# Kernel optimization log

Measured on AMD Instinct MI355X. Metric: run time of the kernel, lower is better.

## Reference

```python
import jax, jax.numpy as jnp
import numpy as np

SEQ_LEN = 2048
EMBED = 1024
HIDDEN = 64
BATCH = 8


def setup_inputs() -> dict:
    key = jax.random.key(0)
    ks = jax.random.split(key, 7)
    s = 1.0 / np.sqrt(EMBED)
    return {
        "inputs": jax.random.normal(ks[0], (BATCH, SEQ_LEN, EMBED), dtype=jnp.float32),
        "Wq": jax.random.uniform(ks[1], (EMBED, HIDDEN), jnp.float32, -s, s),
        "bq": jax.random.uniform(ks[2], (HIDDEN,), jnp.float32, -s, s),
        "Wk": jax.random.uniform(ks[3], (EMBED, HIDDEN), jnp.float32, -s, s),
        "bk": jax.random.uniform(ks[4], (HIDDEN,), jnp.float32, -s, s),
        "Wv": jax.random.uniform(ks[5], (EMBED, HIDDEN), jnp.float32, -s, s),
        "bv": jax.random.uniform(ks[6], (HIDDEN,), jnp.float32, -s, s),
    }


def reference(inputs, Wq, bq, Wk, bk, Wv, bv):
    # inputs: [B, T, E]
    q = inputs @ Wq + bq  # [B, T, H]
    k = inputs @ Wk + bk
    v = inputs @ Wv + bv
    scale = 1.0 / jnp.sqrt(jnp.asarray(k.shape[-1], q.dtype))
    scores = jnp.einsum("bqh,bkh->bqk", q, k) * scale  # [B, T, T]
    T = scores.shape[1]
    tril = jnp.tril(jnp.ones((T, T), dtype=scores.dtype))
    # NOTE: multiplicative mask (zeros out future scores) exactly as in the torch module,
    # NOT an additive -inf mask.
    scores = scores * tril
    attn = jax.nn.softmax(scores, axis=-1)
    return jnp.einsum("bqk,bkh->bqh", attn, v)  # [B, T, H]
```

## Files before the change

kernel.cpp:

```cpp
#include <hip/hip_runtime.h>

#define NBATCH 8
#define TSEQ 2048
#define EDIM 1024
#define HDIM 64
#define NROW (NBATCH * TSEQ)

typedef unsigned short u16;
typedef __attribute__((ext_vector_type(8))) short bf16x8;
typedef __attribute__((ext_vector_type(8))) short short8;
typedef __attribute__((ext_vector_type(4))) float f32x4;

typedef unsigned int uint_as1 __attribute__((address_space(1)));
typedef unsigned int uint_as3 __attribute__((address_space(3)));

__device__ __forceinline__ u16 f2b(float x) {
  unsigned int u = __float_as_uint(x);
  unsigned int r = (u + 0x7fffu + ((u >> 16) & 1u)) >> 16;
  return (u16)r;
}
__device__ __forceinline__ float b2f(u16 h) {
  return __uint_as_float(((unsigned int)h) << 16);
}
__device__ __forceinline__ void gl16(const void* g, void* l) {
  __builtin_amdgcn_global_load_lds((const uint_as1*)g, (uint_as3*)l, 16, 0, 0);
}

__global__ __launch_bounds__(256) void wt_kernel(
    const float* __restrict__ Wq, const float* __restrict__ Wk,
    const float* __restrict__ Wv, u16* __restrict__ Wt) {
  __shared__ float s[64][65];
  const int o = blockIdx.x >> 4, et = blockIdx.x & 15;
  const float* W = (o == 0) ? Wq : (o == 1) ? Wk : Wv;
  const int t = threadIdx.x;
  const int e0 = et * 64;
#pragma unroll
  for (int i = 0; i < 16; i++) {
    int e = i * 4 + (t >> 6), h = t & 63;
    s[e][h] = W[(size_t)(e0 + e) * HDIM + h];
  }
  __syncthreads();
#pragma unroll
  for (int j = 0; j < 16; j++) {
    int h = j * 4 + (t >> 6), e = t & 63;
    Wt[(size_t)(o * 64 + h) * EDIM + e0 + e] = f2b(s[e][h]);
  }
}

#define XBUF (32 * 256)
#define WBUF (192 * 128)

__global__ __launch_bounds__(256, 2) void proj_mfma(
    const float* __restrict__ X, const u16* __restrict__ Wt,
    const float* __restrict__ bq, const float* __restrict__ bk,
    const float* __restrict__ bv,
    u16* __restrict__ Qb, u16* __restrict__ Kb, u16* __restrict__ Vt) {
  __shared__ __align__(16) char sx[2 * XBUF];
  __shared__ __align__(16) char sw[2 * WBUF];

  const int tid = threadIdx.x;
  const int w = tid >> 6, l = tid & 63;
  const int g = l >> 4, li = l & 15;
  const long bt0 = (long)blockIdx.x * 32;

  const int xr = tid >> 4, xc = tid & 15;
  const float* xsrc0 = X + (bt0 + xr) * EDIM + ((xc ^ (xr & 7)) * 4);
  const float* xsrc1 = X + (bt0 + 16 + xr) * EDIM + ((xc ^ (xr & 7)) * 4);

  f32x4 acc[6];
#pragma unroll
  for (int i = 0; i < 6; i++) acc[i] = (f32x4)0.f;

#define STAGE(BUF, E0)                                                       \
  do {                                                                       \
    gl16(xsrc0 + (E0), sx + (BUF)*XBUF + tid * 16);                          \
    gl16(xsrc1 + (E0), sx + (BUF)*XBUF + (tid + 256) * 16);                  \
    _Pragma("unroll") for (int j = 0; j < 6; j++) {                          \
      const int L = j * 256 + tid;                                           \
      const int r = L >> 3, c = L & 7;                                       \
      gl16(Wt + (size_t)r * EDIM + (E0) + ((c ^ (r & 7)) * 8),               \
           sw + (BUF)*WBUF + L * 16);                                        \
    }                                                                        \
  } while (0)

  STAGE(0, 0);
  asm volatile("s_waitcnt vmcnt(0)" ::: "memory");
  __builtin_amdgcn_sched_barrier(0);
  __builtin_amdgcn_s_barrier();
  __builtin_amdgcn_sched_barrier(0);

  for (int ks = 0; ks < 16; ks++) {
    const int buf = ks & 1;
    if (ks < 15) STAGE(buf ^ 1, (ks + 1) * 64);
    __builtin_amdgcn_sched_barrier(0);
    if (ks < 15) {
      asm volatile("s_waitcnt vmcnt(8)" ::: "memory");
    } else {
      asm volatile("s_waitcnt vmcnt(0)" ::: "memory");
    }
    __builtin_amdgcn_sched_barrier(0);
    __builtin_amdgcn_s_barrier();
    __builtin_amdgcn_sched_barrier(0);

    const char* xb = sx + buf * XBUF;
    const char* wb = sw + buf * WBUF;
    bf16x8 bfr[2][2];
#pragma unroll
    for (int cs = 0; cs < 2; cs++) {
      const int row = cs * 16 + li;
#pragma unroll
      for (int kc = 0; kc < 2; kc++) {
        const int G0 = kc * 8 + g * 2;
        const float4 f0 = *(const float4*)(xb + row * 256 + ((G0 ^ (row & 7)) * 16));
        const float4 f1 = *(const float4*)(xb + row * 256 + (((G0 + 1) ^ (row & 7)) * 16));
        bfr[cs][kc] = (bf16x8){(short)f2b(f0.x), (short)f2b(f0.y),
                               (short)f2b(f0.z), (short)f2b(f0.w),
                               (short)f2b(f1.x), (short)f2b(f1.y),
                               (short)f2b(f1.z), (short)f2b(f1.w)};
      }
    }
#pragma unroll
    for (int mt = 0; mt < 3; mt++) {
      const int row = w * 48 + mt * 16 + li;
#pragma unroll
      for (int kc = 0; kc < 2; kc++) {
        const int G = kc * 4 + g;
        const bf16x8 af = *(const bf16x8*)(wb + row * 128 + ((G ^ (row & 7)) * 16));
        acc[mt * 2 + 0] = __builtin_amdgcn_mfma_f32_16x16x32_bf16(
            af, bfr[0][kc], acc[mt * 2 + 0], 0, 0, 0);
        acc[mt * 2 + 1] = __builtin_amdgcn_mfma_f32_16x16x32_bf16(
            af, bfr[1][kc], acc[mt * 2 + 1], 0, 0, 0);
      }
    }
    __builtin_amdgcn_sched_barrier(0);
    __builtin_amdgcn_s_barrier();
    __builtin_amdgcn_sched_barrier(0);
  }
#undef STAGE

  const float qscale = 0.18033688011112042f;
#pragma unroll
  for (int cs = 0; cs < 2; cs++) {
    const long tg = bt0 + cs * 16 + li;
    const int b = (int)(tg >> 11), tl = (int)(tg & 2047);
#pragma unroll
    for (int mt = 0; mt < 3; mt++) {
      const int n0 = w * 48 + mt * 16 + g * 4;
      const int o = n0 >> 6;
      const int h0 = n0 & 63;
      const float* bias = (o == 0) ? bq : (o == 1) ? bk : bv;
      const float4 bb = *(const float4*)&bias[h0];
      const f32x4 a = acc[mt * 2 + cs];
      float v0 = a.x + bb.x, v1 = a.y + bb.y;
      float v2 = a.z + bb.z, v3 = a.w + bb.w;
      if (o == 0) {
        v0 *= qscale; v1 *= qscale; v2 *= qscale; v3 *= qscale;
        uint2 pk = make_uint2((unsigned)f2b(v0) | ((unsigned)f2b(v1) << 16),
                              (unsigned)f2b(v2) | ((unsigned)f2b(v3) << 16));
        *(uint2*)&Qb[tg * HDIM + h0] = pk;
      } else if (o == 1) {
        uint2 pk = make_uint2((unsigned)f2b(v0) | ((unsigned)f2b(v1) << 16),
                              (unsigned)f2b(v2) | ((unsigned)f2b(v3) << 16));
        *(uint2*)&Kb[tg * HDIM + h0] = pk;
      } else {
        Vt[(size_t)(b * 64 + h0 + 0) * TSEQ + tl] = f2b(v0);
        Vt[(size_t)(b * 64 + h0 + 1) * TSEQ + tl] = f2b(v1);
        Vt[(size_t)(b * 64 + h0 + 2) * TSEQ + tl] = f2b(v2);
        Vt[(size_t)(b * 64 + h0 + 3) * TSEQ + tl] = f2b(v3);
      }
    }
  }
}

__global__ __launch_bounds__(1024) void css_kernel(const u16* __restrict__ Vt,
                                                   float* __restrict__ CSS) {
  __shared__ float cs[32][64];
  const int b = blockIdx.x;
  const int t = threadIdx.x;
  const int h = t & 63, cg = t >> 6;
  const u16* vp = Vt + ((size_t)b * 64 + h) * TSEQ + cg * 128;
  float s0 = 0.f, s1 = 0.f;
#pragma unroll
  for (int i = 0; i < 8; i++) {
    const short8 a = *(const short8*)(vp + i * 8);
    s0 += b2f((u16)a[0]) + b2f((u16)a[1]) + b2f((u16)a[2]) + b2f((u16)a[3]) +
          b2f((u16)a[4]) + b2f((u16)a[5]) + b2f((u16)a[6]) + b2f((u16)a[7]);
  }
#pragma unroll
  for (int i = 8; i < 16; i++) {
    const short8 a = *(const short8*)(vp + i * 8);
    s1 += b2f((u16)a[0]) + b2f((u16)a[1]) + b2f((u16)a[2]) + b2f((u16)a[3]) +
          b2f((u16)a[4]) + b2f((u16)a[5]) + b2f((u16)a[6]) + b2f((u16)a[7]);
  }
  cs[cg * 2 + 0][h] = s0;
  cs[cg * 2 + 1][h] = s1;
  __syncthreads();
  if (t < 64) {
    float S = 0.f;
    CSS[((size_t)b * 33 + 32) * 64 + t] = 0.f;
    for (int c = 31; c >= 0; c--) {
      S += cs[c][t];
      CSS[((size_t)b * 33 + c) * 64 + t] = S;
    }
  }
}

#define ISSUE_K(K0A, K1A, KO)                                              \
  do {                                                                     \
    _Pragma("unroll") for (int n = 0; n < 4; n++) {                        \
      const u16* kp_ = Kbb + (size_t)((KO) + n * 16 + li) * HDIM + g * 8;  \
      K0A[n] = *(const bf16x8*)(kp_);                                      \
      K1A[n] = *(const bf16x8*)(kp_ + 32);                                 \
    }                                                                      \
  } while (0)

#define ISSUE_V(KO)                                                        \
  do {                                                                     \
    _Pragma("unroll") for (int n = 0; n < 4; n++) {                        \
      const u16* vp_ = Vtb + (size_t)(n * 16 + li) * TSEQ + (KO) + g * 8;  \
      vf0[n] = *(const bf16x8*)(vp_);                                      \
      vf1[n] = *(const bf16x8*)(vp_ + 32);                                 \
    }                                                                      \
  } while (0)

#define COMPUTE_TILE(K0A, K1A, KO)                                         \
  do {                                                                     \
    f32x4 sA_[4], sB_[4];                                                  \
    _Pragma("unroll") for (int n = 0; n < 4; n++) {                        \
      sA_[n] = (f32x4)0.f;                                                 \
      sA_[n] = __builtin_amdgcn_mfma_f32_16x16x32_bf16(K0A[n], qa0[0], sA_[n], 0, 0, 0); \
      sA_[n] = __builtin_amdgcn_mfma_f32_16x16x32_bf16(K1A[n], qa0[1], sA_[n], 0, 0, 0); \
      sB_[n] = (f32x4)0.f;                                                 \
      sB_[n] = __builtin_amdgcn_mfma_f32_16x16x32_bf16(K0A[n], qa1[0], sB_[n], 0, 0, 0); \
      sB_[n] = __builtin_amdgcn_mfma_f32_16x16x32_bf16(K1A[n], qa1[1], sB_[n], 0, 0, 0); \
    }                                                                      \
    _Pragma("unroll") for (int n = 0; n < 4; n++) {                        \
      const int kb_ = (KO) + n * 16 + g * 4;                               \
      float p0_ = (kb_ + 0 <= qiL0) ? exp2f(sA_[n][0]) : 1.0f;             \
      float p1_ = (kb_ + 1 <= qiL0) ? exp2f(sA_[n][1]) : 1.0f;             \
      float p2_ = (kb_ + 2 <= qiL0) ? exp2f(sA_[n][2]) : 1.0f;             \
      float p3_ = (kb_ + 3 <= qiL0) ? exp2f(sA_[n][3]) : 1.0f;             \
      zaccA += (p0_ + p1_) + (p2_ + p3_);                                  \
      uint2 pk_ = make_uint2((unsigned)f2b(p0_) | ((unsigned)f2b(p1_) << 16), \
                             (unsigned)f2b(p2_) | ((unsigned)f2b(p3_) << 16)); \
      *(uint2*)(sppw + li * 144 + n * 32 + g * 8) = pk_;                   \
      float q0_ = (kb_ + 0 <= qiL1) ? exp2f(sB_[n][0]) : 1.0f;             \
      float q1_ = (kb_ + 1 <= qiL1) ? exp2f(sB_[n][1]) : 1.0f;             \
      float q2_ = (kb_ + 2 <= qiL1) ? exp2f(sB_[n][2]) : 1.0f;             \
      float q3_ = (kb_ + 3 <= qiL1) ? exp2f(sB_[n][3]) : 1.0f;             \
      zaccB += (q0_ + q1_) + (q2_ + q3_);                                  \
      uint2 qk_ = make_uint2((unsigned)f2b(q0_) | ((unsigned)f2b(q1_) << 16), \
                             (unsigned)f2b(q2_) | ((unsigned)f2b(q3_) << 16)); \
      *(uint2*)(sppw + (li + 16) * 144 + n * 32 + g * 8) = qk_;            \
    }                                                                      \
    asm volatile("s_waitcnt lgkmcnt(0)" ::: "memory");                     \
    __builtin_amdgcn_sched_barrier(0);                                     \
    const bf16x8 paA0_ = *(const bf16x8*)(sppw + li * 144 + g * 16);       \
    const bf16x8 paA1_ = *(const bf16x8*)(sppw + li * 144 + 64 + g * 16);  \
    const bf16x8 paB0_ = *(const bf16x8*)(sppw + (li + 16) * 144 + g * 16);\
    const bf16x8 paB1_ = *(const bf16x8*)(sppw + (li + 16) * 144 + 64 + g * 16); \
    _Pragma("unroll") for (int nt = 0; nt < 4; nt++) {                     \
      oaccA[nt] = __builtin_amdgcn_mfma_f32_16x16x32_bf16(paA0_, vf0[nt], oaccA[nt], 0, 0, 0); \
      oaccA[nt] = __builtin_amdgcn_mfma_f32_16x16x32_bf16(paA1_, vf1[nt], oaccA[nt], 0, 0, 0); \
      oaccB[nt] = __builtin_amdgcn_mfma_f32_16x16x32_bf16(paB0_, vf0[nt], oaccB[nt], 0, 0, 0); \
      oaccB[nt] = __builtin_amdgcn_mfma_f32_16x16x32_bf16(paB1_, vf1[nt], oaccB[nt], 0, 0, 0); \
    }                                                                      \
  } while (0)

__global__ __launch_bounds__(256, 2) void attn_mfma(
    const u16* __restrict__ Qb, const u16* __restrict__ Kb,
    const u16* __restrict__ Vt, const float* __restrict__ CSS,
    float* __restrict__ Out) {
  __shared__ __align__(16) u16 spp[4][32][72];
  __shared__ float spm[4][32][68];

  const int tid = threadIdx.x;
  const int w = tid >> 6, l = tid & 63;
  const int g = l >> 4, li = l & 15;

  const int gb = blockIdx.x & 7;
  const int j = blockIdx.x >> 3;
  const int gr = 63 - j;
  const int q0 = gr * 32;
  const int qiL0 = q0 + li;
  const int qiL1 = q0 + 16 + li;

  char* sppw = (char*)&spp[w][0][0];

  const size_t qbase0 = ((size_t)gb * TSEQ + q0 + li) * HDIM;
  bf16x8 qa0[2], qa1[2];
  qa0[0] = *(const bf16x8*)(Qb + qbase0 + g * 8);
  qa0[1] = *(const bf16x8*)(Qb + qbase0 + g * 8 + 32);
  qa1[0] = *(const bf16x8*)(Qb + qbase0 + 16 * HDIM + g * 8);
  qa1[1] = *(const bf16x8*)(Qb + qbase0 + 16 * HDIM + g * 8 + 32);

  float zaccA = 0.f, zaccB = 0.f;
  f32x4 oaccA[4], oaccB[4];
#pragma unroll
  for (int nt = 0; nt < 4; nt++) { oaccA[nt] = (f32x4)0.f; oaccB[nt] = (f32x4)0.f; }

  const int nt = gr / 2 + 1;
  const u16* Kbb = Kb + (size_t)gb * TSEQ * HDIM;
  const u16* Vtb = Vt + (size_t)gb * 64 * TSEQ;

  bf16x8 kA0[4], kA1[4], kB0[4], kB1[4], vf0[4], vf1[4];

  int kt = w;
  if (kt < nt) {
    ISSUE_K(kA0, kA1, kt * 64);
    while (true) {
      ISSUE_V(kt * 64);
      if (kt + 4 < nt) ISSUE_K(kB0, kB1, (kt + 4) * 64);
      __builtin_amdgcn_sched_barrier(0);
      COMPUTE_TILE(kA0, kA1, kt * 64);
      kt += 4;
      if (kt >= nt) break;
      ISSUE_V(kt * 64);
      if (kt + 4 < nt) ISSUE_K(kA0, kA1, (kt + 4) * 64);
      __builtin_amdgcn_sched_barrier(0);
      COMPUTE_TILE(kB0, kB1, kt * 64);
      kt += 4;
      if (kt >= nt) break;
    }
  }

  zaccA += __shfl_xor(zaccA, 16, 64);
  zaccA += __shfl_xor(zaccA, 32, 64);
  zaccB += __shfl_xor(zaccB, 16, 64);
  zaccB += __shfl_xor(zaccB, 32, 64);

#pragma unroll
  for (int n = 0; n < 4; n++) {
#pragma unroll
    for (int r = 0; r < 4; r++) {
      spm[w][g * 4 + r][n * 16 + li] = oaccA[n][r];
      spm[w][16 + g * 4 + r][n * 16 + li] = oaccB[n][r];
    }
  }
  if (l < 16) spm[w][l][64] = zaccA;
  else if (l < 32) spm[w][16 + (l & 15)][64] = zaccB;
  __syncthreads();

  const float tailz = (float)(TSEQ - nt * 64);
  const float tailv = CSS[((size_t)gb * 33 + nt) * 64 + l];
#pragma unroll
  for (int r = 0; r < 8; r++) {
    const int q = w * 8 + r;
    const int qi = q0 + q;
    float a = ((spm[0][q][l] + spm[1][q][l]) + (spm[2][q][l] + spm[3][q][l]));
    float zz = ((spm[0][q][64] + spm[1][q][64]) + (spm[2][q][64] + spm[3][q][64]));
    zz += tailz;
    a += tailv;
    Out[((size_t)gb * TSEQ + qi) * HDIM + l] = a / zz;
  }
}

extern "C" void kernel_launch(void* const* d_in, const int* in_sizes, int n_in,
                              void* d_out, int out_size, void* d_ws, size_t ws_size,
                              hipStream_t stream) {
  const float* X  = (const float*)d_in[0];
  const float* Wq = (const float*)d_in[1];
  const float* bq = (const float*)d_in[2];
  const float* Wk = (const float*)d_in[3];
  const float* bk = (const float*)d_in[4];
  const float* Wv = (const float*)d_in[5];
  const float* bv = (const float*)d_in[6];
  float* out = (float*)d_out;

  char* ws = (char*)d_ws;
  u16*   Qb  = (u16*)(ws);
  u16*   Kb  = (u16*)(ws + 2097152);
  u16*   Vt  = (u16*)(ws + 4194304);
  u16*   Wt  = (u16*)(ws + 6291456);
  float* CSS = (float*)(ws + 6684672);

  wt_kernel<<<48, 256, 0, stream>>>(Wq, Wk, Wv, Wt);
  proj_mfma<<<NROW / 32, 256, 0, stream>>>(X, Wt, bq, bk, bv, Qb, Kb, Vt);
  css_kernel<<<NBATCH, 1024, 0, stream>>>(Vt, CSS);
  attn_mfma<<<512, 256, 0, stream>>>(Qb, Kb, Vt, CSS, out);
}
```

Before: 69.54 us.

## Load projection weights directly into registers instead of staging through LDS

The projection kernel no longer copies the transposed weight tile into shared memory. Each wave now loads its weight fragments straight from global memory into double-buffered registers (wA/wB) one k-step ahead, and only X goes through LDS. The k-loop is fully unrolled and launch bounds are raised to 3 blocks per SM, since the smaller LDS footprint allows higher occupancy. The trade-off is more register pressure and uncoalesced per-lane global reads of weights that LDS previously shared across the block. The vmcnt wait counts were retuned to match the new number of loads in flight.

Result: slower. 75.68 us (+8.8%).

```diff
diff --git a/kernel.cpp b/kernel.cpp
--- a/kernel.cpp
+++ b/kernel.cpp
@@ -48,15 +48,13 @@
 }
 
 #define XBUF (32 * 256)
-#define WBUF (192 * 128)
-
-__global__ __launch_bounds__(256, 2) void proj_mfma(
+
+__global__ __launch_bounds__(256, 3) void proj_mfma(
     const float* __restrict__ X, const u16* __restrict__ Wt,
     const float* __restrict__ bq, const float* __restrict__ bk,
     const float* __restrict__ bv,
     u16* __restrict__ Qb, u16* __restrict__ Kb, u16* __restrict__ Vt) {
   __shared__ __align__(16) char sx[2 * XBUF];
-  __shared__ __align__(16) char sw[2 * WBUF];
 
   const int tid = threadIdx.x;
   const int w = tid >> 6, l = tid & 63;
@@ -67,76 +65,95 @@
   const float* xsrc0 = X + (bt0 + xr) * EDIM + ((xc ^ (xr & 7)) * 4);
   const float* xsrc1 = X + (bt0 + 16 + xr) * EDIM + ((xc ^ (xr & 7)) * 4);
 
+  const u16* Wb = Wt + (size_t)(w * 48 + li) * EDIM + g * 8;
+
   f32x4 acc[6];
 #pragma unroll
   for (int i = 0; i < 6; i++) acc[i] = (f32x4)0.f;
 
-#define STAGE(BUF, E0)                                                       \
+  bf16x8 wA[6], wB[6];
+
+#define PSTG_X(BUF, E0)                                                      \
   do {                                                                       \
     gl16(xsrc0 + (E0), sx + (BUF)*XBUF + tid * 16);                          \
     gl16(xsrc1 + (E0), sx + (BUF)*XBUF + (tid + 256) * 16);                  \
-    _Pragma("unroll") for (int j = 0; j < 6; j++) {                          \
-      const int L = j * 256 + tid;                                           \
-      const int r = L >> 3, c = L & 7;                                       \
-      gl16(Wt + (size_t)r * EDIM + (E0) + ((c ^ (r & 7)) * 8),               \
-           sw + (BUF)*WBUF + L * 16);                                        \
+  } while (0)
+
+#define PISS_W(WS, E0)                                                       \
+  do {                                                                       \
+    _Pragma("unroll") for (int mt = 0; mt < 3; mt++) {                       \
+      _Pragma("unroll") for (int kc = 0; kc < 2; kc++) {                     \
+        WS[mt * 2 + kc] =                                                    \
+            *(const bf16x8*)(Wb + (size_t)mt * 16 * EDIM + (E0) + kc * 32);  \
+      }                                                                      \
     }                                                                        \
   } while (0)
 
-  STAGE(0, 0);
-  asm volatile("s_waitcnt vmcnt(0)" ::: "memory");
+#define PCOMP(WS, XB)                                                        \
+  do {                                                                       \
+    bf16x8 bfr[2][2];                                                        \
+    _Pragma("unroll") for (int cs = 0; cs < 2; cs++) {                       \
+      const int row = cs * 16 + li;                                          \
+      _Pragma("unroll") for (int kc = 0; kc < 2; kc++) {                     \
+        const int G0 = kc * 8 + g * 2;                                       \
+        const float4 f0 =                                                    \
+            *(const float4*)((XB) + row * 256 + ((G0 ^ (row & 7)) * 16));    \
+        const float4 f1 =                                                    \
+            *(const float4*)((XB) + row * 256 + (((G0 + 1) ^ (row & 7)) * 16)); \
+        bfr[cs][kc] = (bf16x8){(short)f2b(f0.x), (short)f2b(f0.y),           \
+                               (short)f2b(f0.z), (short)f2b(f0.w),           \
+                               (short)f2b(f1.x), (short)f2b(f1.y),           \
+                               (short)f2b(f1.z), (short)f2b(f1.w)};          \
+      }                                                                      \
+    }                                                                        \
+    _Pragma("unroll") for (int mt = 0; mt < 3; mt++) {                       \
+      _Pragma("unroll") for (int kc = 0; kc < 2; kc++) {                     \
+        acc[mt * 2 + 0] = __builtin_amdgcn_mfma_f32_16x16x32_bf16(           \
+            WS[mt * 2 + kc], bfr[0][kc], acc[mt * 2 + 0], 0, 0, 0);          \
+        acc[mt * 2 + 1] = __builtin_amdgcn_mfma_f32_16x16x32_bf16(           \
+            WS[mt * 2 + kc], bfr[1][kc], acc[mt * 2 + 1], 0, 0, 0);          \
+      }                                                                      \
+    }                                                                        \
+  } while (0)
+
+  PSTG_X(0, 0);
   __builtin_amdgcn_sched_barrier(0);
-  __builtin_amdgcn_s_barrier();
+  PISS_W(wA, 0);
   __builtin_amdgcn_sched_barrier(0);
 
+#pragma unroll
   for (int ks = 0; ks < 16; ks++) {
     const int buf = ks & 1;
-    if (ks < 15) STAGE(buf ^ 1, (ks + 1) * 64);
-    __builtin_amdgcn_sched_barrier(0);
     if (ks < 15) {
-      asm volatile("s_waitcnt vmcnt(8)" ::: "memory");
+      PSTG_X(buf ^ 1, (ks + 1) * 64);
+      __builtin_amdgcn_sched_barrier(0);
+      if (ks & 1) {
+        PISS_W(wA, (ks + 1) * 64);
+      } else {
+        PISS_W(wB, (ks + 1) * 64);
+      }
+      __builtin_amdgcn_sched_barrier(0);
+      asm volatile("s_waitcnt vmcnt(14)" ::: "memory");
     } else {
-      asm volatile("s_waitcnt vmcnt(0)" ::: "memory");
+      asm volatile("s_waitcnt vmcnt(6)" ::: "memory");
     }
     __builtin_amdgcn_sched_barrier(0);
     __builtin_amdgcn_s_barrier();
     __builtin_amdgcn_sched_barrier(0);
 
     const char* xb = sx + buf * XBUF;
-    const char* wb = sw + buf * WBUF;
-    bf16x8 bfr[2][2];
-#pragma unroll
-    for (int cs = 0; cs < 2; cs++) {
-      const int row = cs * 16 + li;
-#pragma unroll
-      for (int kc = 0; kc < 2; kc++) {
-        const int G0 = kc * 8 + g * 2;
-        const float4 f0 = *(const float4*)(xb + row * 256 + ((G0 ^ (row & 7)) * 16));
-        const float4 f1 = *(const float4*)(xb + row * 256 + (((G0 + 1) ^ (row & 7)) * 16));
-        bfr[cs][kc] = (bf16x8){(short)f2b(f0.x), (short)f2b(f0.y),
-                               (short)f2b(f0.z), (short)f2b(f0.w),
-                               (short)f2b(f1.x), (short)f2b(f1.y),
-                               (short)f2b(f1.z), (short)f2b(f1.w)};
-      }
-    }
-#pragma unroll
-    for (int mt = 0; mt < 3; mt++) {
-      const int row = w * 48 + mt * 16 + li;
-#pragma unroll
-      for (int kc = 0; kc < 2; kc++) {
-        const int G = kc * 4 + g;
-        const bf16x8 af = *(const bf16x8*)(wb + row * 128 + ((G ^ (row & 7)) * 16));
-        acc[mt * 2 + 0] = __builtin_amdgcn_mfma_f32_16x16x32_bf16(
-            af, bfr[0][kc], acc[mt * 2 + 0], 0, 0, 0);
-        acc[mt * 2 + 1] = __builtin_amdgcn_mfma_f32_16x16x32_bf16(
-            af, bfr[1][kc], acc[mt * 2 + 1], 0, 0, 0);
-      }
+    if (ks & 1) {
+      PCOMP(wB, xb);
+    } else {
+      PCOMP(wA, xb);
     }
     __builtin_amdgcn_sched_barrier(0);
     __builtin_amdgcn_s_barrier();
     __builtin_amdgcn_sched_barrier(0);
   }
-#undef STAGE
+#undef PSTG_X
+#undef PISS_W
+#undef PCOMP
 
   const float qscale = 0.18033688011112042f;
 #pragma unroll
```

## Deepen projection pipeline to 4 stages with K=32 tiles; raise MFMA priority

Applied to the files above, without the earlier changes.

The projection kernel's shared-memory staging moves from a double buffer of 64-wide K slices to a four-deep ring of 32-wide slices. Three slices are prefetched ahead, and the next load is issued after the barrier, so more global loads stay in flight per wave. Swizzle patterns and the vmcnt wait counts are adjusted to match. Separately, the attention kernel wraps its MFMA blocks in s_setprio to favour matrix-core issue over the exp/softmax phases of co-resident waves. Halving the K step doubles the number of barriers and loop iterations in the projection.

Measured after the change: 72.69 us. +4.5%, slower.

```diff
diff --git a/kernel.cpp b/kernel.cpp
--- a/kernel.cpp
+++ b/kernel.cpp
@@ -47,25 +47,24 @@
   }
 }
 
-#define XBUF (32 * 256)
-#define WBUF (192 * 128)
+#define XB32 (32 * 128)
+#define WB32 (192 * 64)
 
 __global__ __launch_bounds__(256, 2) void proj_mfma(
     const float* __restrict__ X, const u16* __restrict__ Wt,
     const float* __restrict__ bq, const float* __restrict__ bk,
     const float* __restrict__ bv,
     u16* __restrict__ Qb, u16* __restrict__ Kb, u16* __restrict__ Vt) {
-  __shared__ __align__(16) char sx[2 * XBUF];
-  __shared__ __align__(16) char sw[2 * WBUF];
+  __shared__ __align__(16) char sx[4 * XB32];
+  __shared__ __align__(16) char sw[4 * WB32];
 
   const int tid = threadIdx.x;
   const int w = tid >> 6, l = tid & 63;
   const int g = l >> 4, li = l & 15;
   const long bt0 = (long)blockIdx.x * 32;
 
-  const int xr = tid >> 4, xc = tid & 15;
-  const float* xsrc0 = X + (bt0 + xr) * EDIM + ((xc ^ (xr & 7)) * 4);
-  const float* xsrc1 = X + (bt0 + 16 + xr) * EDIM + ((xc ^ (xr & 7)) * 4);
+  const int xr = tid >> 3, xc = tid & 7;
+  const float* xsrc = X + (bt0 + xr) * EDIM + ((xc ^ (xr & 7)) * 4);
 
   f32x4 acc[6];
 #pragma unroll
@@ -73,28 +72,26 @@
 
 #define STAGE(BUF, E0)                                                       \
   do {                                                                       \
-    gl16(xsrc0 + (E0), sx + (BUF)*XBUF + tid * 16);                          \
-    gl16(xsrc1 + (E0), sx + (BUF)*XBUF + (tid + 256) * 16);                  \
-    _Pragma("unroll") for (int j = 0; j < 6; j++) {                          \
+    gl16(xsrc + (E0), sx + (BUF)*XB32 + tid * 16);                           \
+    _Pragma("unroll") for (int j = 0; j < 3; j++) {                          \
       const int L = j * 256 + tid;                                           \
-      const int r = L >> 3, c = L & 7;                                       \
-      gl16(Wt + (size_t)r * EDIM + (E0) + ((c ^ (r & 7)) * 8),               \
-           sw + (BUF)*WBUF + L * 16);                                        \
+      const int r = L >> 2, c = L & 3;                                       \
+      gl16(Wt + (size_t)r * EDIM + (E0) + ((c ^ (r & 3)) * 8),               \
+           sw + (BUF)*WB32 + L * 16);                                        \
     }                                                                        \
   } while (0)
 
   STAGE(0, 0);
-  asm volatile("s_waitcnt vmcnt(0)" ::: "memory");
-  __builtin_amdgcn_sched_barrier(0);
-  __builtin_amdgcn_s_barrier();
-  __builtin_amdgcn_sched_barrier(0);
-
-  for (int ks = 0; ks < 16; ks++) {
-    const int buf = ks & 1;
-    if (ks < 15) STAGE(buf ^ 1, (ks + 1) * 64);
-    __builtin_amdgcn_sched_barrier(0);
-    if (ks < 15) {
+  STAGE(1, 32);
+  STAGE(2, 64);
+
+  for (int ks = 0; ks < 32; ks++) {
+    const int buf = ks & 3;
+    __builtin_amdgcn_sched_barrier(0);
+    if (ks <= 29) {
       asm volatile("s_waitcnt vmcnt(8)" ::: "memory");
+    } else if (ks == 30) {
+      asm volatile("s_waitcnt vmcnt(4)" ::: "memory");
     } else {
       asm volatile("s_waitcnt vmcnt(0)" ::: "memory");
     }
@@ -102,39 +99,32 @@
     __builtin_amdgcn_s_barrier();
     __builtin_amdgcn_sched_barrier(0);
 
-    const char* xb = sx + buf * XBUF;
-    const char* wb = sw + buf * WBUF;
-    bf16x8 bfr[2][2];
+    const char* xb = sx + buf * XB32;
+    const char* wb = sw + buf * WB32;
+    bf16x8 bfr[2];
 #pragma unroll
     for (int cs = 0; cs < 2; cs++) {
       const int row = cs * 16 + li;
-#pragma unroll
-      for (int kc = 0; kc < 2; kc++) {
-        const int G0 = kc * 8 + g * 2;
-        const float4 f0 = *(const float4*)(xb + row * 256 + ((G0 ^ (row & 7)) * 16));
-        const float4 f1 = *(const float4*)(xb + row * 256 + (((G0 + 1) ^ (row & 7)) * 16));
-        bfr[cs][kc] = (bf16x8){(short)f2b(f0.x), (short)f2b(f0.y),
-                               (short)f2b(f0.z), (short)f2b(f0.w),
-                               (short)f2b(f1.x), (short)f2b(f1.y),
-                               (short)f2b(f1.z), (short)f2b(f1.w)};
-      }
+      const float4 f0 = *(const float4*)(xb + row * 128 + (((g * 2) ^ (row & 7)) * 16));
+      const float4 f1 = *(const float4*)(xb + row * 128 + (((g * 2 + 1) ^ (row & 7)) * 16));
+      bfr[cs] = (bf16x8){(short)f2b(f0.x), (short)f2b(f0.y),
+                         (short)f2b(f0.z), (short)f2b(f0.w),
+                         (short)f2b(f1.x), (short)f2b(f1.y),
+                         (short)f2b(f1.z), (short)f2b(f1.w)};
     }
 #pragma unroll
     for (int mt = 0; mt < 3; mt++) {
       const int row = w * 48 + mt * 16 + li;
-#pragma unroll
-      for (int kc = 0; kc < 2; kc++) {
-        const int G = kc * 4 + g;
-        const bf16x8 af = *(const bf16x8*)(wb + row * 128 + ((G ^ (row & 7)) * 16));
-        acc[mt * 2 + 0] = __builtin_amdgcn_mfma_f32_16x16x32_bf16(
-            af, bfr[0][kc], acc[mt * 2 + 0], 0, 0, 0);
-        acc[mt * 2 + 1] = __builtin_amdgcn_mfma_f32_16x16x32_bf16(
-            af, bfr[1][kc], acc[mt * 2 + 1], 0, 0, 0);
-      }
+      const bf16x8 af = *(const bf16x8*)(wb + row * 64 + ((g ^ (row & 3)) * 16));
+      acc[mt * 2 + 0] = __builtin_amdgcn_mfma_f32_16x16x32_bf16(
+          af, bfr[0], acc[mt * 2 + 0], 0, 0, 0);
+      acc[mt * 2 + 1] = __builtin_amdgcn_mfma_f32_16x16x32_bf16(
+          af, bfr[1], acc[mt * 2 + 1], 0, 0, 0);
     }
     __builtin_amdgcn_sched_barrier(0);
     __builtin_amdgcn_s_barrier();
     __builtin_amdgcn_sched_barrier(0);
+    if (ks <= 28) STAGE((ks + 3) & 3, (ks + 3) * 32);
   }
 #undef STAGE
 
@@ -226,6 +216,7 @@
 #define COMPUTE_TILE(K0A, K1A, KO)                                         \
   do {                                                                     \
     f32x4 sA_[4], sB_[4];                                                  \
+    __builtin_amdgcn_s_setprio(1);                                         \
     _Pragma("unroll") for (int n = 0; n < 4; n++) {                        \
       sA_[n] = (f32x4)0.f;                                                 \
       sA_[n] = __builtin_amdgcn_mfma_f32_16x16x32_bf16(K0A[n], qa0[0], sA_[n], 0, 0, 0); \
@@ -234,6 +225,7 @@
       sB_[n] = __builtin_amdgcn_mfma_f32_16x16x32_bf16(K0A[n], qa1[0], sB_[n], 0, 0, 0); \
       sB_[n] = __builtin_amdgcn_mfma_f32_16x16x32_bf16(K1A[n], qa1[1], sB_[n], 0, 0, 0); \
     }                                                                      \
+    __builtin_amdgcn_s_setprio(0);                                         \
     _Pragma("unroll") for (int n = 0; n < 4; n++) {                        \
       const int kb_ = (KO) + n * 16 + g * 4;                               \
       float p0_ = (kb_ + 0 <= qiL0) ? exp2f(sA_[n][0]) : 1.0f;             \
@@ -259,12 +251,14 @@
     const bf16x8 paA1_ = *(const bf16x8*)(sppw + li * 144 + 64 + g * 16);  \
     const bf16x8 paB0_ = *(const bf16x8*)(sppw + (li + 16) * 144 + g * 16);\
     const bf16x8 paB1_ = *(const bf16x8*)(sppw + (li + 16) * 144 + 64 + g * 16); \
+    __builtin_amdgcn_s_setprio(1);                                         \
     _Pragma("unroll") for (int nt = 0; nt < 4; nt++) {                     \
       oaccA[nt] = __builtin_amdgcn_mfma_f32_16x16x32_bf16(paA0_, vf0[nt], oaccA[nt], 0, 0, 0); \
       oaccA[nt] = __builtin_amdgcn_mfma_f32_16x16x32_bf16(paA1_, vf1[nt], oaccA[nt], 0, 0, 0); \
       oaccB[nt] = __builtin_amdgcn_mfma_f32_16x16x32_bf16(paB0_, vf0[nt], oaccB[nt], 0, 0, 0); \
       oaccB[nt] = __builtin_amdgcn_mfma_f32_16x16x32_bf16(paB1_, vf1[nt], oaccB[nt], 0, 0, 0); \
     }                                                                      \
+    __builtin_amdgcn_s_setprio(0);                                         \
   } while (0)
 
 __global__ __launch_bounds__(256, 2) void attn_mfma(
```
